# Kernel tuning notes

Hardware: AMD Instinct MI355X
Metric: run time of the kernel (lower is better)

## Reference

```python
import jax, jax.numpy as jnp
import numpy as np

N = 65536      # active voxels
K = 27         # 3x3x3 SubM kernel taps
CIN = 4        # input voxel features (x,y,z,intensity)
C = 32         # stage-1 channels
NW = 2048      # number of attention windows
CAP = 32       # padded voxels per window (NW*CAP == N)
H = 2          # attention heads
HD = C // H    # head dim
R = 144        # quantized relative-position bins


def _subm_conv(feats, pairs, w):
    # spconv SubMConv3d as gather-scatter: pairs[k, i] = input voxel feeding
    # kernel tap k of output voxel i, or -1 if that neighbor is empty.
    valid = pairs >= 0                      # [K, N]
    idx = jnp.where(valid, pairs, 0)
    g = feats[idx] * valid[:, :, None].astype(feats.dtype)   # [K, N, Cin]
    return jnp.einsum('knc,kcd->nd', g, w)                    # [N, Cout]


def _bn_relu(x, g, b):
    # BatchNorm1d (eval, running stats folded) + ReLU
    return jax.nn.relu(x * g + b)


def _res_block(x, pairs, g1, b1, w1, g2, b2, w2):
    h = _bn_relu(x, g1, b1)
    h = _subm_conv(h, pairs, w1)
    h = _bn_relu(h, g2, b2)
    h = _subm_conv(h, pairs, w2)
    return x + h  # identity branch (in_ch == out_ch)


def _sphere_attention(x, win_idx, rel_idx, w_qkv, b_qkv, w_proj, b_proj, tq, tk, tv):
    xw = x[win_idx]                                           # [NW, CAP, C]
    qkv = (xw @ w_qkv + b_qkv).reshape(NW, CAP, 3, H, HD)
    q = qkv[:, :, 0] * (HD ** -0.5)
    k = qkv[:, :, 1]
    v = qkv[:, :, 2]
    scores = jnp.einsum('wihd,wjhd->whij', q, k)              # [NW, H, CAP, CAP]
    # quantized relative-position contributions (rel_query / rel_key)
    rq = tq[rel_idx]                                          # [NW, CAP, CAP, H, HD]
    rk = tk[rel_idx]
    scores = scores + jnp.einsum('wihd,wijhd->whij', q, rq)
    scores = scores + jnp.einsum('wjhd,wijhd->whij', k, rk)
    attn = jax.nn.softmax(scores, axis=-1)
    out = jnp.einsum('whij,wjhd->wihd', attn, v)
    out = out + jnp.einsum('whij,wijhd->wihd', attn, tv[rel_idx])  # rel_value
    out = out.reshape(NW, CAP, C) @ w_proj + b_proj
    # scatter windows back to the flat voxel list (win_idx is a permutation)
    y = jnp.zeros_like(x).at[win_idx.reshape(-1)].set(out.reshape(-1, C))
    return x + y  # residual (drop_path=0 in stage 1)


def setup_inputs() -> dict:
    key = jax.random.key(0)
    ks = jax.random.split(key, 16)
    feats = jax.random.normal(ks[0], (N, CIN), dtype=jnp.float32)
    pairs = jax.random.randint(ks[1], (K, N), 0, N, dtype=jnp.int32)
    drop = jax.random.uniform(ks[2], (K, N)) < 0.3
    pairs = jnp.where(drop, -1, pairs)
    pairs = pairs.at[K // 2].set(jnp.arange(N, dtype=jnp.int32))  # center tap = self
    win_idx = jax.random.permutation(ks[3], N).reshape(NW, CAP).astype(jnp.int32)
    rel_idx = jax.random.randint(ks[4], (NW, CAP, CAP), 0, R, dtype=jnp.int32)

    def w(k, shape, s=0.05):
        return jax.random.normal(k, shape, dtype=jnp.float32) * s

    wk = jax.random.split(ks[5], 12)
    inp = dict(feats=feats, pairs=pairs, win_idx=win_idx, rel_idx=rel_idx,
               w_in=w(wk[0], (K, CIN, C)),
               rb1_g1=jnp.ones((C,)), rb1_b1=jnp.zeros((C,)), rb1_w1=w(wk[1], (K, C, C)),
               rb1_g2=jnp.ones((C,)), rb1_b2=jnp.zeros((C,)), rb1_w2=w(wk[2], (K, C, C)),
               rb2_g1=jnp.ones((C,)), rb2_b1=jnp.zeros((C,)), rb2_w1=w(wk[3], (K, C, C)),
               rb2_g2=jnp.ones((C,)), rb2_b2=jnp.zeros((C,)), rb2_w2=w(wk[4], (K, C, C)),
               w_qkv=w(wk[5], (C, 3 * C), 0.1), b_qkv=jnp.zeros((3 * C,)),
               w_proj=w(wk[6], (C, C), 0.1), b_proj=jnp.zeros((C,)),
               tq=w(wk[7], (R, H, HD)), tk=w(wk[8], (R, H, HD)), tv=w(wk[9], (R, H, HD)))
    return inp


def reference(feats, pairs, win_idx, rel_idx, w_in,
              rb1_g1, rb1_b1, rb1_w1, rb1_g2, rb1_b2, rb1_w2,
              rb2_g1, rb2_b1, rb2_w1, rb2_g2, rb2_b2, rb2_w2,
              w_qkv, b_qkv, w_proj, b_proj, tq, tk, tv):
    x = _subm_conv(feats, pairs, w_in)                       # input_conv
    x = _res_block(x, pairs, rb1_g1, rb1_b1, rb1_w1, rb1_g2, rb1_b2, rb1_w2)
    x = _res_block(x, pairs, rb2_g1, rb2_b1, rb2_w1, rb2_g2, rb2_b2, rb2_w2)
    x = _sphere_attention(x, win_idx, rel_idx, w_qkv, b_qkv, w_proj, b_proj, tq, tk, tv)
    return x
```

## Files before the change

kernel.cpp:

```cpp
#include <hip/hip_runtime.h>

typedef unsigned short u16;
typedef unsigned int u32;

#define N_PTS 65536
#define KK 27
#define CIN 4
#define CC 32
#define NWIN 2048
#define CAP 32
#define NH 2
#define HD 16

typedef short s16x8 __attribute__((ext_vector_type(8)));
typedef float f32x4 __attribute__((ext_vector_type(4)));

__device__ __forceinline__ float bf2f(u16 h) { return __uint_as_float(((u32)h) << 16); }
__device__ __forceinline__ u16 f2bf(float f) {
    u32 u = __float_as_uint(f);
    u32 r = (u + 0x7FFFu + ((u >> 16) & 1u)) >> 16;
    return (u16)r;
}
__device__ __forceinline__ float ldany(const void* src, int i, bool isbf) {
    return isbf ? bf2f(((const u16*)src)[i]) : ((const float*)src)[i];
}
__device__ __forceinline__ u16 ldbf(const void* src, int i, bool isbf) {
    return isbf ? ((const u16*)src)[i] : f2bf(((const float*)src)[i]);
}
__device__ __forceinline__ void unp8(uint4 u, float* f) {
    f[0] = __uint_as_float(u.x << 16); f[1] = __uint_as_float(u.x & 0xffff0000u);
    f[2] = __uint_as_float(u.y << 16); f[3] = __uint_as_float(u.y & 0xffff0000u);
    f[4] = __uint_as_float(u.z << 16); f[5] = __uint_as_float(u.z & 0xffff0000u);
    f[6] = __uint_as_float(u.w << 16); f[7] = __uint_as_float(u.w & 0xffff0000u);
}

__global__ void detect_kernel(const u32* __restrict__ w, int* flag) {
    int t = threadIdx.x;
    int cnt = 0;
    for (int i = t; i < 4096; i += 256) {
        u32 e = (w[i] >> 7) & 0xFFu;
        cnt += (e >= 100 && e <= 140) ? 1 : 0;
    }
    __shared__ int red[256];
    red[t] = cnt;
    __syncthreads();
    for (int s = 128; s > 0; s >>= 1) {
        if (t < s) red[t] += red[t + s];
        __syncthreads();
    }
    if (t == 0) flag[0] = (red[0] > 2048) ? 1 : 0;
}

struct Ptrs { const void* p[24]; };

__global__ __launch_bounds__(256) void prep_all(
    Ptrs in, const int* __restrict__ flag,
    u16* __restrict__ fbf,
    u16* __restrict__ WpA1, u16* __restrict__ WpA2,
    u16* __restrict__ WpB1, u16* __restrict__ WpB2, u16* __restrict__ WpIN,
    u16* __restrict__ wqkvB, u16* __restrict__ wprojB,
    u16* __restrict__ tqb, u16* __restrict__ tkb, u16* __restrict__ tvb,
    float* __restrict__ Pf)
{
    bool isbf = flag[0] != 0;
    int seg = blockIdx.y;
    int i = blockIdx.x * 256 + threadIdx.x;
    if (seg == 0) {
        if (i < N_PTS * CIN) fbf[i] = ldbf(in.p[0], i, isbf);
        return;
    }
    if (seg <= 4) {
        if (i < 27648) {
            int e = i & 7, l = (i >> 3) & 63, dt = (i >> 9) & 1, k = i >> 10;
            const void* src = in.p[seg == 1 ? 7 : seg == 2 ? 10 : seg == 3 ? 13 : 16];
            u16* dst = seg == 1 ? WpA1 : seg == 2 ? WpA2 : seg == 3 ? WpB1 : WpB2;
            dst[i] = ldbf(src, k * 1024 + ((l >> 4) * 8 + e) * 32 + dt * 16 + (l & 15), isbf);
        }
        return;
    }
    if (seg == 5) {
        if (i < 4096) {
            int e = i & 7, l = (i >> 3) & 63, dt = (i >> 9) & 1, kk = i >> 10;
            int g = kk * 32 + (l >> 4) * 8 + e;
            int tp = g >> 2, c = g & 3;
            WpIN[i] = (tp < KK) ? ldbf(in.p[4], tp * 128 + c * 32 + dt * 16 + (l & 15), isbf) : (u16)0;
        }
        return;
    }
    if (seg == 6) {
        if (i < 3072) {
            int e = i & 7, l = (i >> 3) & 63, n = i >> 9;
            wqkvB[i] = ldbf(in.p[17], ((l >> 4) * 8 + e) * 96 + n * 16 + (l & 15), isbf);
        } else if (i < 4096) {
            int o2 = i - 3072;
            int e = o2 & 7, l = (o2 >> 3) & 63, n = o2 >> 9;
            wprojB[o2] = ldbf(in.p[19], ((l >> 4) * 8 + e) * 32 + n * 16 + (l & 15), isbf);
        }
        return;
    }
    if (seg == 7) {
        if (i < 4608)            tqb[i] = ldbf(in.p[21], i, isbf);
        else if (i < 9216)       tkb[i - 4608] = ldbf(in.p[22], i - 4608, isbf);
        else if (i < 13824)      tvb[i - 9216] = ldbf(in.p[23], i - 9216, isbf);
        return;
    }
    if (i < 256) {
        const int srcs[8] = {5, 6, 8, 9, 11, 12, 14, 15};
        Pf[i] = ldany(in.p[srcs[i >> 5]], i & 31, isbf);
    } else if (i < 352) {
        Pf[i] = ldany(in.p[18], i - 256, isbf);
    } else if (i < 384) {
        Pf[i] = ldany(in.p[20], i - 352, isbf);
    }
}

__global__ __launch_bounds__(256) void convin_mfma(
    const u16* __restrict__ fb, const int* __restrict__ pairs,
    const u16* __restrict__ Wp, const float* __restrict__ gb,
    float* __restrict__ xbuf, u16* __restrict__ act_out)
{
    int t = threadIdx.x;
    int wv = t >> 6, l = t & 63;
    int lr = l & 15, lg = l >> 4;
    int p0 = (blockIdx.x * 4 + wv) * 16;
    int rowaddr = p0 + lr;

    f32x4 acc0 = {0.f, 0.f, 0.f, 0.f}, acc1 = {0.f, 0.f, 0.f, 0.f};
#pragma unroll
    for (int kk = 0; kk < 4; kk++) {
        int t0 = kk * 8 + lg * 2;
        int ta = t0 < 26 ? t0 : 26;
        int tb = (t0 + 1) < 26 ? (t0 + 1) : 26;
        int ia = pairs[ta * N_PTS + rowaddr];
        int ib = pairs[tb * N_PTS + rowaddr];
        u32 ma = (t0 < KK && ia >= 0) ? 0xFFFFFFFFu : 0u;
        u32 mb = (t0 + 1 < KK && ib >= 0) ? 0xFFFFFFFFu : 0u;
        uint2 qa = *(const uint2*)(fb + (long)(ia < 0 ? 0 : ia) * CIN);
        uint2 qb = *(const uint2*)(fb + (long)(ib < 0 ? 0 : ib) * CIN);
        union { uint4 q; s16x8 v; } a;
        a.q = make_uint4(qa.x & ma, qa.y & ma, qb.x & mb, qb.y & mb);
        const s16x8* wb = (const s16x8*)Wp + kk * 128 + l;
        s16x8 b0 = wb[0];
        s16x8 b1 = wb[64];
        acc0 = __builtin_amdgcn_mfma_f32_16x16x32_bf16(a.v, b0, acc0, 0, 0, 0);
        acc1 = __builtin_amdgcn_mfma_f32_16x16x32_bf16(a.v, b1, acc1, 0, 0, 0);
    }
    float g0 = gb[lr], b0v = gb[32 + lr], g1 = gb[16 + lr], b1v = gb[48 + lr];
#pragma unroll
    for (int r = 0; r < 4; r++) {
        int row = p0 + lg * 4 + r;
        long o0 = (long)row * 32 + lr, o1 = o0 + 16;
        float v0 = acc0[r], v1 = acc1[r];
        xbuf[o0] = v0; xbuf[o1] = v1;
        act_out[o0] = f2bf(fmaxf(fmaf(v0, g0, b0v), 0.f));
        act_out[o1] = f2bf(fmaxf(fmaf(v1, g1, b1v), 0.f));
    }
}

template <int M>
__global__ __launch_bounds__(256) void conv32_mfma(
    const u16* __restrict__ act_in, const int* __restrict__ pairs,
    const u16* __restrict__ Wp, const float* __restrict__ gb,
    float* __restrict__ xbuf, u16* __restrict__ act_out)
{
    int t = threadIdx.x;
    int wv = t >> 6, l = t & 63;
    int lr = l & 15, lg = l >> 4;
    int p0 = (blockIdx.x * 4 + wv) * 16;
    int rowaddr = p0 + lr;

    int idx[KK];
#pragma unroll
    for (int k = 0; k < KK; k++) idx[k] = pairs[k * N_PTS + rowaddr];

    f32x4 acc0 = {0.f, 0.f, 0.f, 0.f}, acc1 = {0.f, 0.f, 0.f, 0.f};
#pragma unroll
    for (int k = 0; k < KK; k++) {
        const s16x8* wb = (const s16x8*)Wp + k * 128 + l;
        s16x8 b0 = wb[0];
        s16x8 b1 = wb[64];
        int ic = idx[k] < 0 ? 0 : idx[k];
        uint4 q = *(const uint4*)(act_in + (long)ic * CC + lg * 8);
        u32 msk = idx[k] >= 0 ? 0xFFFFFFFFu : 0u;
        q.x &= msk; q.y &= msk; q.z &= msk; q.w &= msk;
        union { uint4 q; s16x8 v; } a;
        a.q = q;
        acc0 = __builtin_amdgcn_mfma_f32_16x16x32_bf16(a.v, b0, acc0, 0, 0, 0);
        acc1 = __builtin_amdgcn_mfma_f32_16x16x32_bf16(a.v, b1, acc1, 0, 0, 0);
    }
    float g0 = 0.f, b0v = 0.f, g1 = 0.f, b1v = 0.f;
    if (M & 4) { g0 = gb[lr]; b0v = gb[32 + lr]; g1 = gb[16 + lr]; b1v = gb[48 + lr]; }
#pragma unroll
    for (int r = 0; r < 4; r++) {
        int row = p0 + lg * 4 + r;
        long o0 = (long)row * 32 + lr, o1 = o0 + 16;
        float v0 = acc0[r], v1 = acc1[r];
        if (M & 1) { v0 += xbuf[o0]; v1 += xbuf[o1]; }
        if (M & 2) { xbuf[o0] = v0; xbuf[o1] = v1; }
        if (M & 4) {
            act_out[o0] = f2bf(fmaxf(fmaf(v0, g0, b0v), 0.f));
            act_out[o1] = f2bf(fmaxf(fmaf(v1, g1, b1v), 0.f));
        }
    }
}

__global__ __launch_bounds__(256) void attn3_kernel(
    const float* __restrict__ x, const int* __restrict__ win_idx,
    const int* __restrict__ rel_idx,
    const u16* __restrict__ wqkvB, const u16* __restrict__ wprojB,
    const float* __restrict__ Pf,
    const u16* __restrict__ tqb, const u16* __restrict__ tkb, const u16* __restrict__ tvb,
    float* __restrict__ out)
{
    __shared__ float xw[CAP][CC + 1];
    __shared__ u16 qsb[CAP][40];
    __shared__ u16 ksb[CAP][40];
    __shared__ u16 vsT[CC][40];
    __shared__ float sc[NH][CAP][36];
    __shared__ float ot[CAP][36];
    __shared__ int ridx[CAP * CAP];
    __shared__ int widx[CAP];

    int w = blockIdx.x, t = threadIdx.x;
    int wv = t >> 6, l = t & 63, lr = l & 15, lg = l >> 4;

    if (t < CAP) widx[t] = win_idx[w * CAP + t];
    __syncthreads();

    for (int e = t; e < CAP * CC; e += 256) {
        int i = e >> 5, c = e & 31;
        xw[i][c] = x[(long)widx[i] * CC + c];
        ridx[e] = rel_idx[(long)w * CAP * CAP + e];
    }
    __syncthreads();

    {
        const float* bqkv = Pf + 256;
        for (int pi = wv; pi < 12; pi += 4) {
            int n = pi >> 1, m = pi & 1;
            union { s16x8 v; u16 h[8]; } a;
            const float* xr = &xw[m * 16 + lr][0];
#pragma unroll
            for (int e = 0; e < 8; e++) a.h[e] = f2bf(xr[lg * 8 + e]);
            s16x8 b = *(const s16x8*)(wqkvB + ((n * 64 + l) << 3));
            f32x4 acc = {0.f, 0.f, 0.f, 0.f};
            acc = __builtin_amdgcn_mfma_f32_16x16x32_bf16(a.v, b, acc, 0, 0, 0);
            int tt = n * 16 + lr;
            float bias = bqkv[tt];
#pragma unroll
            for (int r = 0; r < 4; r++) {
                int tok = m * 16 + lg * 4 + r;
                float v = acc[r] + bias;
                if (tt < 32)      qsb[tok][tt] = f2bf(v * 0.25f);
                else if (tt < 64) ksb[tok][tt - 32] = f2bf(v);
                else              vsT[tt - 64][tok] = f2bf(v);
            }
        }
    }
    __syncthreads();

    for (int pi = wv; pi < 8; pi += 4) {
        int h = pi >> 2, m = (pi >> 1) & 1, n = pi & 1;
        s16x8 a = {0, 0, 0, 0, 0, 0, 0, 0}, b = {0, 0, 0, 0, 0, 0, 0, 0};
        if (lg < 2) {
            a = *(const s16x8*)(&qsb[m * 16 + lr][h * 16 + lg * 8]);
            b = *(const s16x8*)(&ksb[n * 16 + lr][h * 16 + lg * 8]);
        }
        f32x4 acc = {0.f, 0.f, 0.f, 0.f};
        acc = __builtin_amdgcn_mfma_f32_16x16x32_bf16(a, b, acc, 0, 0, 0);
#pragma unroll
        for (int r = 0; r < 4; r++)
            sc[h][m * 16 + lg * 4 + r][n * 16 + lr] = acc[r];
    }
    __syncthreads();

    for (int e = t; e < NH * CAP * CAP; e += 256) {
        int h = e >> 10, i = (e >> 5) & 31, j = e & 31;
        int r = ridx[i * 32 + j];
        float qf[16], kf[16], tf[16], uf[16];
        unp8(*(const uint4*)(&qsb[i][h * 16]), qf);
        unp8(*(const uint4*)(&qsb[i][h * 16 + 8]), qf + 8);
        unp8(*(const uint4*)(&ksb[j][h * 16]), kf);
        unp8(*(const uint4*)(&ksb[j][h * 16 + 8]), kf + 8);
        unp8(*(const uint4*)(tqb + r * 32 + h * 16), tf);
        unp8(*(const uint4*)(tqb + r * 32 + h * 16 + 8), tf + 8);
        unp8(*(const uint4*)(tkb + r * 32 + h * 16), uf);
        unp8(*(const uint4*)(tkb + r * 32 + h * 16 + 8), uf + 8);
        float s = sc[h][i][j];
#pragma unroll
        for (int d = 0; d < 16; d++) {
            s = fmaf(qf[d], tf[d], s);
            s = fmaf(kf[d], uf[d], s);
        }
        sc[h][i][j] = s;
    }
    __syncthreads();

    {
        int rr = t >> 2, sub = t & 3;
        int h = rr >> 5, i = rr & 31, j0 = sub * 8;
        float pv[8];
        float m = -1e30f;
#pragma unroll
        for (int jj = 0; jj < 8; jj++) { pv[jj] = sc[h][i][j0 + jj]; m = fmaxf(m, pv[jj]); }
        m = fmaxf(m, __shfl_xor(m, 1));
        m = fmaxf(m, __shfl_xor(m, 2));
        float sum = 0.f;
#pragma unroll
        for (int jj = 0; jj < 8; jj++) { pv[jj] = __expf(pv[jj] - m); sum += pv[jj]; }
        sum += __shfl_xor(sum, 1);
        sum += __shfl_xor(sum, 2);
        float inv = 1.f / sum;
#pragma unroll
        for (int jj = 0; jj < 8; jj++) sc[h][i][j0 + jj] = pv[jj] * inv;
    }
    __syncthreads();

    for (int o = t; o < CAP * 16; o += 256) {
        int i = o >> 4, hp = o & 15;
        int h = hp >> 3;
        float a0 = 0.f, a1 = 0.f;
#pragma unroll 8
        for (int j = 0; j < CAP; j++) {
            int r = ridx[i * 32 + j];
            float p = sc[h][i][j];
            u32 tv2 = *(const u32*)(tvb + r * 32 + hp * 2);
            a0 = fmaf(p, __uint_as_float(tv2 << 16), a0);
            a1 = fmaf(p, __uint_as_float(tv2 & 0xffff0000u), a1);
        }
        ot[i][hp * 2] = a0;
        ot[i][hp * 2 + 1] = a1;
    }
    __syncthreads();

    {
        int h = wv >> 1, m = wv & 1;
        union { s16x8 v; u16 hh[8]; } pa;
        const float* pr = &sc[h][m * 16 + lr][0];
#pragma unroll
        for (int e = 0; e < 8; e++) pa.hh[e] = f2bf(pr[lg * 8 + e]);
        s16x8 b = *(const s16x8*)(&vsT[h * 16 + lr][lg * 8]);
        f32x4 acc = {0.f, 0.f, 0.f, 0.f};
        acc = __builtin_amdgcn_mfma_f32_16x16x32_bf16(pa.v, b, acc, 0, 0, 0);
#pragma unroll
        for (int r = 0; r < 4; r++)
            ot[m * 16 + lg * 4 + r][h * 16 + lr] += acc[r];
    }
    __syncthreads();

    {
        int m = wv >> 1, n = wv & 1;
        union { s16x8 v; u16 hh[8]; } a;
        const float* orow = &ot[m * 16 + lr][0];
#pragma unroll
        for (int e = 0; e < 8; e++) a.hh[e] = f2bf(orow[lg * 8 + e]);
        s16x8 b = *(const s16x8*)(wprojB + ((n * 64 + l) << 3));
        f32x4 acc = {0.f, 0.f, 0.f, 0.f};
        acc = __builtin_amdgcn_mfma_f32_16x16x32_bf16(a.v, b, acc, 0, 0, 0);
        int c = n * 16 + lr;
        float bb = Pf[352 + c];
#pragma unroll
        for (int r = 0; r < 4; r++) {
            int tok = m * 16 + lg * 4 + r;
            out[(long)widx[tok] * CC + c] = xw[tok][c] + bb + acc[r];
        }
    }
}

#define B_PF     0
#define B_FLAG   1536
#define B_ACTA   2048
#define B_ACTB   4196352
#define B_FEATS  8390656
#define B_WA1    8914944
#define B_WA2    8970240
#define B_WB1    9025536
#define B_WB2    9080832
#define B_WIN    9136128
#define B_WQKVB  9144320
#define B_WPROJB 9150464
#define B_TQB    9152512
#define B_TKB    9161728
#define B_TVB    9170944

extern "C" void kernel_launch(void* const* d_in, const int* in_sizes, int n_in,
                              void* d_out, int out_size, void* d_ws, size_t ws_size,
                              hipStream_t stream) {
    const void* feats  = d_in[0];
    const int* pairs   = (const int*)d_in[1];
    const int* win_idx = (const int*)d_in[2];
    const int* rel_idx = (const int*)d_in[3];

    char* wsb = (char*)d_ws;
    float* Pf = (float*)(wsb + B_PF);
    int* flag = (int*)(wsb + B_FLAG);
    u16* actA = (u16*)(wsb + B_ACTA);
    u16* actB = (u16*)(wsb + B_ACTB);
    u16* fbf  = (u16*)(wsb + B_FEATS);
    u16* WpA1 = (u16*)(wsb + B_WA1);
    u16* WpA2 = (u16*)(wsb + B_WA2);
    u16* WpB1 = (u16*)(wsb + B_WB1);
    u16* WpB2 = (u16*)(wsb + B_WB2);
    u16* WpIN = (u16*)(wsb + B_WIN);
    u16* wqkvB  = (u16*)(wsb + B_WQKVB);
    u16* wprojB = (u16*)(wsb + B_WPROJB);
    u16* tqb = (u16*)(wsb + B_TQB);
    u16* tkb = (u16*)(wsb + B_TKB);
    u16* tvb = (u16*)(wsb + B_TVB);
    float* X  = (float*)d_out;

    detect_kernel<<<1, 256, 0, stream>>>((const u32*)feats, flag);

    Ptrs pp;
    for (int i = 0; i < 24; i++) pp.p[i] = d_in[i];
    prep_all<<<dim3(1024, 9), 256, 0, stream>>>(pp, flag, fbf,
                                                WpA1, WpA2, WpB1, WpB2, WpIN,
                                                wqkvB, wprojB, tqb, tkb, tvb, Pf);

    convin_mfma<<<1024, 256, 0, stream>>>(fbf, pairs, WpIN, Pf + 0, X, actA);
    conv32_mfma<4><<<1024, 256, 0, stream>>>(actA, pairs, WpA1, Pf + 64,  X, actB);
    conv32_mfma<7><<<1024, 256, 0, stream>>>(actB, pairs, WpA2, Pf + 128, X, actA);
    conv32_mfma<4><<<1024, 256, 0, stream>>>(actA, pairs, WpB1, Pf + 192, X, actB);
    conv32_mfma<3><<<1024, 256, 0, stream>>>(actB, pairs, WpB2, Pf, X, actA);

    attn3_kernel<<<NWIN, 256, 0, stream>>>(X, win_idx, rel_idx,
                                           wqkvB, wprojB, Pf,
                                           tqb, tkb, tvb, X);
}
```

Before: 136.2 us.

## Precompute per-bin q/k relative-table dot products with MFMA and prefetch conv gathers

The attention kernel no longer computes the 16-dim relative query and key dot products for every (i,j) pair. It first computes q·tq[r] and k·tk[r] for all 144 bins with MFMA into shared tables and then looks them up by rel_idx, with the tq/tk tables pre-laid out in MFMA B-fragment format. It also reads window features straight from global memory instead of staging them in LDS, stores softmax probabilities as bf16 in a reused shared arena, and adds an 8-deep register prefetch ring for the gathered activations in the sparse conv kernels. The tradeoffs are extra MFMA work per window (144 bins versus 32 tokens), bf16 rounding of the intermediate bias terms, and higher register pressure in the conv kernels.

Result: no change. 135.2 us (-0.7%).

```diff
diff --git a/kernel.cpp b/kernel.cpp
--- a/kernel.cpp
+++ b/kernel.cpp
@@ -27,12 +27,6 @@
 __device__ __forceinline__ u16 ldbf(const void* src, int i, bool isbf) {
     return isbf ? ((const u16*)src)[i] : f2bf(((const float*)src)[i]);
 }
-__device__ __forceinline__ void unp8(uint4 u, float* f) {
-    f[0] = __uint_as_float(u.x << 16); f[1] = __uint_as_float(u.x & 0xffff0000u);
-    f[2] = __uint_as_float(u.y << 16); f[3] = __uint_as_float(u.y & 0xffff0000u);
-    f[4] = __uint_as_float(u.z << 16); f[5] = __uint_as_float(u.z & 0xffff0000u);
-    f[6] = __uint_as_float(u.w << 16); f[7] = __uint_as_float(u.w & 0xffff0000u);
-}
 
 __global__ void detect_kernel(const u32* __restrict__ w, int* flag) {
     int t = threadIdx.x;
@@ -59,7 +53,7 @@
     u16* __restrict__ WpA1, u16* __restrict__ WpA2,
     u16* __restrict__ WpB1, u16* __restrict__ WpB2, u16* __restrict__ WpIN,
     u16* __restrict__ wqkvB, u16* __restrict__ wprojB,
-    u16* __restrict__ tqb, u16* __restrict__ tkb, u16* __restrict__ tvb,
+    u16* __restrict__ tqB, u16* __restrict__ tkB, u16* __restrict__ tvb,
     float* __restrict__ Pf)
 {
     bool isbf = flag[0] != 0;
@@ -99,9 +93,21 @@
         return;
     }
     if (seg == 7) {
-        if (i < 4608)            tqb[i] = ldbf(in.p[21], i, isbf);
-        else if (i < 9216)       tkb[i - 4608] = ldbf(in.p[22], i - 4608, isbf);
-        else if (i < 13824)      tvb[i - 9216] = ldbf(in.p[23], i - 9216, isbf);
+        if (i < 9216) {
+            int e = i & 7, l = (i >> 3) & 63, nn = i >> 9;
+            int n = nn % 9, h = nn / 9, lr = l & 15, lg = l >> 4;
+            int k = lg * 8 + e;
+            tqB[i] = (k < HD) ? ldbf(in.p[21], (n * 16 + lr) * 32 + h * 16 + k, isbf) : (u16)0;
+        } else if (i < 18432) {
+            int o2 = i - 9216;
+            int e = o2 & 7, l = (o2 >> 3) & 63, nn = o2 >> 9;
+            int n = nn % 9, h = nn / 9, lr = l & 15, lg = l >> 4;
+            int k = lg * 8 + e;
+            tkB[o2] = (k < HD) ? ldbf(in.p[22], (n * 16 + lr) * 32 + h * 16 + k, isbf) : (u16)0;
+        } else if (i < 23040) {
+            int o2 = i - 18432;
+            tvb[o2] = ldbf(in.p[23], o2, isbf);
+        }
         return;
     }
     if (i < 256) {
@@ -173,18 +179,29 @@
 #pragma unroll
     for (int k = 0; k < KK; k++) idx[k] = pairs[k * N_PTS + rowaddr];
 
+    uint4 qb[8];
+#pragma unroll
+    for (int k = 0; k < 8; k++) {
+        int ic = idx[k] < 0 ? 0 : idx[k];
+        qb[k] = *(const uint4*)(act_in + (long)ic * CC + lg * 8);
+    }
+
     f32x4 acc0 = {0.f, 0.f, 0.f, 0.f}, acc1 = {0.f, 0.f, 0.f, 0.f};
 #pragma unroll
     for (int k = 0; k < KK; k++) {
-        const s16x8* wb = (const s16x8*)Wp + k * 128 + l;
-        s16x8 b0 = wb[0];
-        s16x8 b1 = wb[64];
-        int ic = idx[k] < 0 ? 0 : idx[k];
-        uint4 q = *(const uint4*)(act_in + (long)ic * CC + lg * 8);
+        uint4 q = qb[k & 7];
+        if (k + 8 < KK) {
+            int kn = k + 8;
+            int ic = idx[kn] < 0 ? 0 : idx[kn];
+            qb[kn & 7] = *(const uint4*)(act_in + (long)ic * CC + lg * 8);
+        }
         u32 msk = idx[k] >= 0 ? 0xFFFFFFFFu : 0u;
         q.x &= msk; q.y &= msk; q.z &= msk; q.w &= msk;
         union { uint4 q; s16x8 v; } a;
         a.q = q;
+        const s16x8* wb = (const s16x8*)Wp + k * 128 + l;
+        s16x8 b0 = wb[0];
+        s16x8 b1 = wb[64];
         acc0 = __builtin_amdgcn_mfma_f32_16x16x32_bf16(a.v, b0, acc0, 0, 0, 0);
         acc1 = __builtin_amdgcn_mfma_f32_16x16x32_bf16(a.v, b1, acc1, 0, 0, 0);
     }
@@ -204,44 +221,52 @@
     }
 }
 
-__global__ __launch_bounds__(256) void attn3_kernel(
+#define A5_RIDX 0
+#define A5_QSB  4096
+#define A5_KSB  6656
+#define A5_VST  9216
+#define A5_SC   11776
+#define A5_BQ   20992
+#define A5_BK   30208
+#define A5_SIZE 39424
+
+__global__ __launch_bounds__(256) void attn5_kernel(
     const float* __restrict__ x, const int* __restrict__ win_idx,
     const int* __restrict__ rel_idx,
     const u16* __restrict__ wqkvB, const u16* __restrict__ wprojB,
     const float* __restrict__ Pf,
-    const u16* __restrict__ tqb, const u16* __restrict__ tkb, const u16* __restrict__ tvb,
+    const u16* __restrict__ tqB, const u16* __restrict__ tkB, const u16* __restrict__ tvb,
     float* __restrict__ out)
 {
-    __shared__ float xw[CAP][CC + 1];
-    __shared__ u16 qsb[CAP][40];
-    __shared__ u16 ksb[CAP][40];
-    __shared__ u16 vsT[CC][40];
-    __shared__ float sc[NH][CAP][36];
-    __shared__ float ot[CAP][36];
-    __shared__ int ridx[CAP * CAP];
-    __shared__ int widx[CAP];
+    __shared__ __align__(16) char arena[A5_SIZE];
+    int*   ridx = (int*)(arena + A5_RIDX);
+    u16*   qsb  = (u16*)(arena + A5_QSB);
+    u16*   ksb  = (u16*)(arena + A5_KSB);
+    u16*   vsT  = (u16*)(arena + A5_VST);
+    float* sc   = (float*)(arena + A5_SC);
+    u16*   psb  = (u16*)(arena + A5_SC);
+    u16*   Bq   = (u16*)(arena + A5_BQ);
+    u16*   Bk   = (u16*)(arena + A5_BK);
+    float* ot   = (float*)(arena + A5_BQ);
 
     int w = blockIdx.x, t = threadIdx.x;
     int wv = t >> 6, l = t & 63, lr = l & 15, lg = l >> 4;
 
-    if (t < CAP) widx[t] = win_idx[w * CAP + t];
-    __syncthreads();
-
-    for (int e = t; e < CAP * CC; e += 256) {
-        int i = e >> 5, c = e & 31;
-        xw[i][c] = x[(long)widx[i] * CC + c];
-        ridx[e] = rel_idx[(long)w * CAP * CAP + e];
-    }
-    __syncthreads();
-
+    {
+        int4 r4 = *(const int4*)(rel_idx + (long)w * 1024 + t * 4);
+        *(int4*)(ridx + t * 4) = r4;
+    }
     {
         const float* bqkv = Pf + 256;
         for (int pi = wv; pi < 12; pi += 4) {
             int n = pi >> 1, m = pi & 1;
+            int gi = win_idx[w * 32 + m * 16 + lr];
+            const float* xr = x + (long)gi * 32 + lg * 8;
+            float4 x0 = *(const float4*)(xr);
+            float4 x1 = *(const float4*)(xr + 4);
             union { s16x8 v; u16 h[8]; } a;
-            const float* xr = &xw[m * 16 + lr][0];
-#pragma unroll
-            for (int e = 0; e < 8; e++) a.h[e] = f2bf(xr[lg * 8 + e]);
+            a.h[0] = f2bf(x0.x); a.h[1] = f2bf(x0.y); a.h[2] = f2bf(x0.z); a.h[3] = f2bf(x0.w);
+            a.h[4] = f2bf(x1.x); a.h[5] = f2bf(x1.y); a.h[6] = f2bf(x1.z); a.h[7] = f2bf(x1.w);
             s16x8 b = *(const s16x8*)(wqkvB + ((n * 64 + l) << 3));
             f32x4 acc = {0.f, 0.f, 0.f, 0.f};
             acc = __builtin_amdgcn_mfma_f32_16x16x32_bf16(a.v, b, acc, 0, 0, 0);
@@ -251,109 +276,113 @@
             for (int r = 0; r < 4; r++) {
                 int tok = m * 16 + lg * 4 + r;
                 float v = acc[r] + bias;
-                if (tt < 32)      qsb[tok][tt] = f2bf(v * 0.25f);
-                else if (tt < 64) ksb[tok][tt - 32] = f2bf(v);
-                else              vsT[tt - 64][tok] = f2bf(v);
+                if (tt < 32)      qsb[tok * 40 + tt] = f2bf(v * 0.25f);
+                else if (tt < 64) ksb[tok * 40 + (tt - 32)] = f2bf(v);
+                else              vsT[(tt - 64) * 40 + tok] = f2bf(v);
             }
         }
     }
     __syncthreads();
+
+    for (int h = 0; h < NH; h++) {
+        for (int pi = wv; pi < 36; pi += 4) {
+            int tb = pi >= 18 ? 1 : 0;
+            int rem = pi - tb * 18;
+            int m = rem / 9, n = rem % 9;
+            const u16* src = tb ? ksb : qsb;
+            const u16* tab = tb ? tkB : tqB;
+            s16x8 a = {0, 0, 0, 0, 0, 0, 0, 0};
+            if (lg < 2) a = *(const s16x8*)(src + (m * 16 + lr) * 40 + h * 16 + lg * 8);
+            s16x8 b = *(const s16x8*)(tab + (((h * 9 + n) * 64 + l) << 3));
+            f32x4 acc = {0.f, 0.f, 0.f, 0.f};
+            acc = __builtin_amdgcn_mfma_f32_16x16x32_bf16(a, b, acc, 0, 0, 0);
+            u16* dst = tb ? Bk : Bq;
+#pragma unroll
+            for (int r = 0; r < 4; r++)
+                dst[(m * 16 + lg * 4 + r) * 144 + n * 16 + lr] = f2bf(acc[r]);
+        }
+        __syncthreads();
+        for (int e = t; e < 1024; e += 256) {
+            int i = e >> 5, j = e & 31, r = ridx[e];
+            sc[h * 1152 + i * 36 + j] = bf2f(Bq[i * 144 + r]) + bf2f(Bk[j * 144 + r]);
+        }
+        __syncthreads();
+    }
 
     for (int pi = wv; pi < 8; pi += 4) {
         int h = pi >> 2, m = (pi >> 1) & 1, n = pi & 1;
         s16x8 a = {0, 0, 0, 0, 0, 0, 0, 0}, b = {0, 0, 0, 0, 0, 0, 0, 0};
         if (lg < 2) {
-            a = *(const s16x8*)(&qsb[m * 16 + lr][h * 16 + lg * 8]);
-            b = *(const s16x8*)(&ksb[n * 16 + lr][h * 16 + lg * 8]);
+            a = *(const s16x8*)(qsb + (m * 16 + lr) * 40 + h * 16 + lg * 8);
+            b = *(const s16x8*)(ksb + (n * 16 + lr) * 40 + h * 16 + lg * 8);
         }
         f32x4 acc = {0.f, 0.f, 0.f, 0.f};
         acc = __builtin_amdgcn_mfma_f32_16x16x32_bf16(a, b, acc, 0, 0, 0);
 #pragma unroll
         for (int r = 0; r < 4; r++)
-            sc[h][m * 16 + lg * 4 + r][n * 16 + lr] = acc[r];
-    }
-    __syncthreads();
-
-    for (int e = t; e < NH * CAP * CAP; e += 256) {
-        int h = e >> 10, i = (e >> 5) & 31, j = e & 31;
-        int r = ridx[i * 32 + j];
-        float qf[16], kf[16], tf[16], uf[16];
-        unp8(*(const uint4*)(&qsb[i][h * 16]), qf);
-        unp8(*(const uint4*)(&qsb[i][h * 16 + 8]), qf + 8);
-        unp8(*(const uint4*)(&ksb[j][h * 16]), kf);
-        unp8(*(const uint4*)(&ksb[j][h * 16 + 8]), kf + 8);
-        unp8(*(const uint4*)(tqb + r * 32 + h * 16), tf);
-        unp8(*(const uint4*)(tqb + r * 32 + h * 16 + 8), tf + 8);
-        unp8(*(const uint4*)(tkb + r * 32 + h * 16), uf);
-        unp8(*(const uint4*)(tkb + r * 32 + h * 16 + 8), uf + 8);
-        float s = sc[h][i][j];
-#pragma unroll
-        for (int d = 0; d < 16; d++) {
-            s = fmaf(qf[d], tf[d], s);
-            s = fmaf(kf[d], uf[d], s);
-        }
-        sc[h][i][j] = s;
+            sc[h * 1152 + (m * 16 + lg * 4 + r) * 36 + n * 16 + lr] += acc[r];
     }
     __syncthreads();
 
     {
         int rr = t >> 2, sub = t & 3;
         int h = rr >> 5, i = rr & 31, j0 = sub * 8;
+        const float* srow = sc + h * 1152 + i * 36 + j0;
         float pv[8];
-        float m = -1e30f;
-#pragma unroll
-        for (int jj = 0; jj < 8; jj++) { pv[jj] = sc[h][i][j0 + jj]; m = fmaxf(m, pv[jj]); }
-        m = fmaxf(m, __shfl_xor(m, 1));
-        m = fmaxf(m, __shfl_xor(m, 2));
+        float m_ = -1e30f;
+#pragma unroll
+        for (int jj = 0; jj < 8; jj++) { pv[jj] = srow[jj]; m_ = fmaxf(m_, pv[jj]); }
+        m_ = fmaxf(m_, __shfl_xor(m_, 1));
+        m_ = fmaxf(m_, __shfl_xor(m_, 2));
         float sum = 0.f;
 #pragma unroll
-        for (int jj = 0; jj < 8; jj++) { pv[jj] = __expf(pv[jj] - m); sum += pv[jj]; }
+        for (int jj = 0; jj < 8; jj++) { pv[jj] = __expf(pv[jj] - m_); sum += pv[jj]; }
         sum += __shfl_xor(sum, 1);
         sum += __shfl_xor(sum, 2);
         float inv = 1.f / sum;
-#pragma unroll
-        for (int jj = 0; jj < 8; jj++) sc[h][i][j0 + jj] = pv[jj] * inv;
+        __syncthreads();
+        u16* prow = psb + h * 1280 + i * 40 + j0;
+#pragma unroll
+        for (int jj = 0; jj < 8; jj++) prow[jj] = f2bf(pv[jj] * inv);
     }
     __syncthreads();
 
     for (int o = t; o < CAP * 16; o += 256) {
-        int i = o >> 4, hp = o & 15;
-        int h = hp >> 3;
+        int i = o >> 4, hp = o & 15, h = hp >> 3;
+        const u16* prow = psb + h * 1280 + i * 40;
+        const int* rrow = ridx + i * 32;
         float a0 = 0.f, a1 = 0.f;
 #pragma unroll 8
         for (int j = 0; j < CAP; j++) {
-            int r = ridx[i * 32 + j];
-            float p = sc[h][i][j];
+            int r = rrow[j];
+            float p = bf2f(prow[j]);
             u32 tv2 = *(const u32*)(tvb + r * 32 + hp * 2);
             a0 = fmaf(p, __uint_as_float(tv2 << 16), a0);
             a1 = fmaf(p, __uint_as_float(tv2 & 0xffff0000u), a1);
         }
-        ot[i][hp * 2] = a0;
-        ot[i][hp * 2 + 1] = a1;
+        ot[i * 36 + hp * 2] = a0;
+        ot[i * 36 + hp * 2 + 1] = a1;
     }
     __syncthreads();
 
     {
         int h = wv >> 1, m = wv & 1;
-        union { s16x8 v; u16 hh[8]; } pa;
-        const float* pr = &sc[h][m * 16 + lr][0];
-#pragma unroll
-        for (int e = 0; e < 8; e++) pa.hh[e] = f2bf(pr[lg * 8 + e]);
-        s16x8 b = *(const s16x8*)(&vsT[h * 16 + lr][lg * 8]);
+        s16x8 a = *(const s16x8*)(psb + h * 1280 + (m * 16 + lr) * 40 + lg * 8);
+        s16x8 b = *(const s16x8*)(vsT + (h * 16 + lr) * 40 + lg * 8);
         f32x4 acc = {0.f, 0.f, 0.f, 0.f};
-        acc = __builtin_amdgcn_mfma_f32_16x16x32_bf16(pa.v, b, acc, 0, 0, 0);
+        acc = __builtin_amdgcn_mfma_f32_16x16x32_bf16(a, b, acc, 0, 0, 0);
 #pragma unroll
         for (int r = 0; r < 4; r++)
-            ot[m * 16 + lg * 4 + r][h * 16 + lr] += acc[r];
+            ot[(m * 16 + lg * 4 + r) * 36 + h * 16 + lr] += acc[r];
     }
     __syncthreads();
 
     {
         int m = wv >> 1, n = wv & 1;
-        union { s16x8 v; u16 hh[8]; } a;
-        const float* orow = &ot[m * 16 + lr][0];
-#pragma unroll
-        for (int e = 0; e < 8; e++) a.hh[e] = f2bf(orow[lg * 8 + e]);
+        union { s16x8 v; u16 h[8]; } a;
+        const float* orow = ot + (m * 16 + lr) * 36 + lg * 8;
+#pragma unroll
+        for (int e = 0; e < 8; e++) a.h[e] = f2bf(orow[e]);
         s16x8 b = *(const s16x8*)(wprojB + ((n * 64 + l) << 3));
         f32x4 acc = {0.f, 0.f, 0.f, 0.f};
         acc = __builtin_amdgcn_mfma_f32_16x16x32_bf16(a.v, b, acc, 0, 0, 0);
@@ -362,7 +391,8 @@
 #pragma unroll
         for (int r = 0; r < 4; r++) {
             int tok = m * 16 + lg * 4 + r;
-            out[(long)widx[tok] * CC + c] = xw[tok][c] + bb + acc[r];
+            int gi = win_idx[w * 32 + tok];
+            out[(long)gi * 32 + c] = x[(long)gi * 32 + c] + bb + acc[r];
         }
     }
 }
@@ -379,9 +409,9 @@
 #define B_WIN    9136128
 #define B_WQKVB  9144320
 #define B_WPROJB 9150464
-#define B_TQB    9152512
-#define B_TKB    9161728
-#define B_TVB    9170944
+#define B_TQBF   9152512
+#define B_TKBF   9170944
+#define B_TVBF   9189376
 
 extern "C" void kernel_launch(void* const* d_in, const int* in_sizes, int n_in,
                               void* d_out, int out_size, void* d_ws, size_t ws_size,
@@ -404,9 +434,9 @@
     u16* WpIN = (u16*)(wsb + B_WIN);
     u16* wqkvB  = (u16*)(wsb + B_WQKVB);
     u16* wprojB = (u16*)(wsb + B_WPROJB);
-    u16* tqb = (u16*)(wsb + B_TQB);
-    u16* tkb = (u16*)(wsb + B_TKB);
-    u16* tvb = (u16*)(wsb + B_TVB);
+    u16* tqB = (u16*)(wsb + B_TQBF);
+    u16* tkB = (u16*)(wsb + B_TKBF);
+    u16* tvb = (u16*)(wsb + B_TVBF);
     float* X  = (float*)d_out;
 
     detect_kernel<<<1, 256, 0, stream>>>((const u32*)feats, flag);
@@ -415,7 +445,7 @@
     for (int i = 0; i < 24; i++) pp.p[i] = d_in[i];
     prep_all<<<dim3(1024, 9), 256, 0, stream>>>(pp, flag, fbf,
                                                 WpA1, WpA2, WpB1, WpB2, WpIN,
-                                                wqkvB, wprojB, tqb, tkb, tvb, Pf);
+                                                wqkvB, wprojB, tqB, tkB, tvb, Pf);
 
     convin_mfma<<<1024, 256, 0, stream>>>(fbf, pairs, WpIN, Pf + 0, X, actA);
     conv32_mfma<4><<<1024, 256, 0, stream>>>(actA, pairs, WpA1, Pf + 64,  X, actB);
@@ -423,7 +453,7 @@
     conv32_mfma<4><<<1024, 256, 0, stream>>>(actA, pairs, WpB1, Pf + 192, X, actB);
     conv32_mfma<3><<<1024, 256, 0, stream>>>(actB, pairs, WpB2, Pf, X, actA);
 
-    attn3_kernel<<<NWIN, 256, 0, stream>>>(X, win_idx, rel_idx,
+    attn5_kernel<<<NWIN, 256, 0, stream>>>(X, win_idx, rel_idx,
                                            wqkvB, wprojB, Pf,
-                                           tqb, tkb, tvb, X);
-}
+                                           tqB, tkB, tvb, X);
+}
```
